# Kernel tuning notes

Measured on AMD Instinct MI355X. Metric: run time of the kernel, lower is better.

Reference implementation:

```python
import jax, jax.numpy as jnp
import numpy as np


def gcn_conv(x, src, dst, W, b, num_nodes):
    """PyG GCNConv: out = D^{-1/2} (A+I) D^{-1/2} X W + b (self-loops already in src/dst)."""
    h = x @ W  # [N, F_out]
    ones = jnp.ones(dst.shape[0], dtype=x.dtype)
    deg = jax.ops.segment_sum(ones, dst, num_segments=num_nodes)  # in-degree incl self-loop
    dis = jnp.where(deg > 0, jax.lax.rsqrt(deg), jnp.zeros_like(deg))  # deg^{-1/2}
    norm = dis[src] * dis[dst]  # [E]
    msg = h[src] * norm[:, None]  # gather + scale, [E, F_out]
    out = jax.ops.segment_sum(msg, dst, num_segments=num_nodes) + b
    return out


def setup_inputs() -> dict:
    key = jax.random.key(0)
    k = jax.random.split(key, 6)
    N, E, F_IN, HID, C = 100000, 3200000, 128, 16, 8
    x = jax.random.normal(k[0], (N, F_IN), dtype=jnp.float32)
    edge_index = jax.random.randint(k[1], (2, E), 0, N, dtype=jnp.int64)
    W1 = jax.random.normal(k[2], (F_IN, HID), dtype=jnp.float32) * (1.0 / np.sqrt(F_IN))
    b1 = jnp.zeros((HID,), dtype=jnp.float32)
    W2 = jax.random.normal(k[3], (HID, C), dtype=jnp.float32) * (1.0 / np.sqrt(HID))
    b2 = jnp.zeros((C,), dtype=jnp.float32)
    return {"x": x, "edge_index": edge_index, "W1": W1, "b1": b1, "W2": W2, "b2": b2}


def reference(x, edge_index, W1, b1, W2, b2):
    N = x.shape[0]
    loop = jnp.arange(N, dtype=edge_index.dtype)
    src = jnp.concatenate([edge_index[0], loop])  # add self-loops
    dst = jnp.concatenate([edge_index[1], loop])
    h = gcn_conv(x, src, dst, W1, b1, N)
    h = jax.nn.relu(h)  # dropout is identity in eval mode
    out = gcn_conv(h, src, dst, W2, b2, N)
    return out
```

## Files before the change

kernel.cpp:

```cpp
#include <hip/hip_runtime.h>
#include <hip/hip_fp16.h>

#define F_IN 128
#define HID 16
#define C_OUT 8
#define BSH 6
#define BSZ 64
#define G1 1024
#define NBMAX 1600
#define CAP 3072

typedef unsigned int uint;

__device__ inline int chunk_of_block(int blk) {
    return ((blk & 7) << 7) | (blk >> 3);
}

__global__ void count_kernel(const int* __restrict__ dst, uint* __restrict__ counts,
                             int E, int CE, int NB) {
    __shared__ uint h[NBMAX];
    int chunk = chunk_of_block(blockIdx.x), tid = threadIdx.x;
    for (int i = tid; i < NB; i += 256) h[i] = 0;
    __syncthreads();
    int base = chunk * CE, end = min(E, base + CE);
    int n = end - base;
    if (n > 0) {
        int n4 = n >> 2;
        const int4* p = reinterpret_cast<const int4*>(dst + base);
        for (int i = tid; i < n4; i += 256) {
            int4 d = p[i];
            atomicAdd(&h[((uint)d.x) >> BSH], 1u);
            atomicAdd(&h[((uint)d.y) >> BSH], 1u);
            atomicAdd(&h[((uint)d.z) >> BSH], 1u);
            atomicAdd(&h[((uint)d.w) >> BSH], 1u);
        }
        for (int i = base + (n4 << 2) + tid; i < end; i += 256)
            atomicAdd(&h[((uint)dst[i]) >> BSH], 1u);
    }
    __syncthreads();
    for (int i = tid; i < NB; i += 256)
        counts[(size_t)i * G1 + chunk] = h[i];
}

__global__ void scanA_kernel(uint* __restrict__ counts, uint* __restrict__ btot) {
    int b = blockIdx.x, tid = threadIdx.x;
    int lane = tid & 63, wid = tid >> 6;
    uint v = counts[(size_t)b * G1 + tid];
    uint inc = v;
#pragma unroll
    for (int o = 1; o < 64; o <<= 1) {
        uint t = __shfl_up(inc, o);
        if (lane >= o) inc += t;
    }
    __shared__ uint wsum[16];
    if (lane == 63) wsum[wid] = inc;
    __syncthreads();
    if (tid < 16) {
        uint w = wsum[tid], iw = w;
#pragma unroll
        for (int o = 1; o < 16; o <<= 1) {
            uint t = __shfl_up(iw, o);
            if (tid >= o) iw += t;
        }
        wsum[tid] = iw - w;
        if (tid == 15) btot[b] = iw;
    }
    __syncthreads();
    counts[(size_t)b * G1 + tid] = wsum[wid] + inc - v;
}

__global__ void scanB_kernel(const uint* __restrict__ btot, uint* __restrict__ bbase,
                             int NB, int E) {
    __shared__ uint wsum[4];
    __shared__ uint ctot;
    int tid = threadIdx.x, lane = tid & 63, wid = tid >> 6;
    uint base = 0;
    for (int c0 = 0; c0 < NB; c0 += 256) {
        int i = c0 + tid;
        uint v = (i < NB) ? btot[i] : 0u;
        uint inc = v;
#pragma unroll
        for (int o = 1; o < 64; o <<= 1) {
            uint t = __shfl_up(inc, o);
            if (lane >= o) inc += t;
        }
        if (lane == 63) wsum[wid] = inc;
        __syncthreads();
        if (tid == 0) {
            uint s = 0;
#pragma unroll
            for (int k = 0; k < 4; ++k) { uint t = wsum[k]; wsum[k] = s; s += t; }
            ctot = s;
        }
        __syncthreads();
        if (i < NB) bbase[i] = base + wsum[wid] + inc - v;
        base += ctot;
        __syncthreads();
    }
    if (tid == 0) bbase[NB] = (uint)E;
}

__global__ void place_kernel(const int* __restrict__ src, const int* __restrict__ dst,
                             const uint* __restrict__ offs, const uint* __restrict__ bbase,
                             uint* __restrict__ rec, int E, int CE, int NB) {
    __shared__ uint cur[NBMAX];
    int chunk = chunk_of_block(blockIdx.x), tid = threadIdx.x;
    for (int i = tid; i < NB; i += 256)
        cur[i] = bbase[i] + offs[(size_t)i * G1 + chunk];
    __syncthreads();
    int base = chunk * CE, end = min(E, base + CE);
    int n = end - base;
    if (n <= 0) return;
    int n4 = n >> 2;
    const int4* ps = reinterpret_cast<const int4*>(src + base);
    const int4* pd = reinterpret_cast<const int4*>(dst + base);
    for (int i = tid; i < n4; i += 256) {
        int4 s = ps[i];
        int4 d = pd[i];
        uint p0 = atomicAdd(&cur[((uint)d.x) >> BSH], 1u);
        rec[p0] = (uint)s.x | (((uint)d.x & (BSZ - 1)) << 17);
        uint p1 = atomicAdd(&cur[((uint)d.y) >> BSH], 1u);
        rec[p1] = (uint)s.y | (((uint)d.y & (BSZ - 1)) << 17);
        uint p2 = atomicAdd(&cur[((uint)d.z) >> BSH], 1u);
        rec[p2] = (uint)s.z | (((uint)d.z & (BSZ - 1)) << 17);
        uint p3 = atomicAdd(&cur[((uint)d.w) >> BSH], 1u);
        rec[p3] = (uint)s.w | (((uint)d.w & (BSZ - 1)) << 17);
    }
    for (int i = base + (n4 << 2) + tid; i < end; i += 256) {
        int d = dst[i];
        uint b = ((uint)d) >> BSH;
        uint p = atomicAdd(&cur[b], 1u);
        rec[p] = (uint)src[i] | (((uint)d & (BSZ - 1)) << 17);
    }
}

__global__ void sortdis_kernel(uint* __restrict__ rec, const uint* __restrict__ bbase,
                               uint* __restrict__ nstart, float* __restrict__ dis,
                               int N, int NB) {
    __shared__ uint tmp[CAP];
    __shared__ uint h[BSZ];
    __shared__ uint cur[BSZ];
    int b = blockIdx.x, tid = threadIdx.x;
    if (tid < BSZ) h[tid] = 0;
    uint s0 = bbase[b], s1 = bbase[b + 1];
    uint seg = min(s1 - s0, (uint)CAP);
    __syncthreads();
    for (uint i = tid; i < seg; i += 256) {
        uint r = rec[s0 + i];
        tmp[i] = r;
        atomicAdd(&h[(r >> 17) & (BSZ - 1)], 1u);
    }
    __syncthreads();
    if (tid < BSZ) {
        uint v = h[tid], inc = v;
#pragma unroll
        for (int o = 1; o < BSZ; o <<= 1) {
            uint t = __shfl_up(inc, o);
            if (tid >= o) inc += t;
        }
        uint excl = inc - v;
        cur[tid] = s0 + excl;
        int n = b * BSZ + tid;
        if (n < N) {
            nstart[n] = s0 + excl;
            dis[n] = rsqrtf((float)v + 1.0f);
        }
    }
    if (b == NB - 1 && tid == 0) nstart[N] = s1;
    __syncthreads();
    for (uint i = tid; i < seg; i += 256) {
        uint r = tmp[i];
        uint p = atomicAdd(&cur[(r >> 17) & (BSZ - 1)], 1u);
        rec[p] = r & 0x1FFFFu;
    }
}

__global__ void h1_kernel(const float* __restrict__ x, const float* __restrict__ W1,
                          const float* __restrict__ dis, __half* __restrict__ hs1, int N) {
    __shared__ float w[F_IN * HID];
    for (int t = threadIdx.x; t < F_IN * HID; t += blockDim.x) w[t] = W1[t];
    __syncthreads();
    int row = blockIdx.x * blockDim.x + threadIdx.x;
    if (row >= N) return;
    float acc[HID];
#pragma unroll
    for (int j = 0; j < HID; ++j) acc[j] = 0.f;
    const float4* xr = reinterpret_cast<const float4*>(x + (size_t)row * F_IN);
#pragma unroll 4
    for (int k4 = 0; k4 < F_IN / 4; ++k4) {
        float4 v = xr[k4];
        int k = k4 * 4;
#pragma unroll
        for (int j = 0; j < HID; ++j) {
            acc[j] += v.x * w[(k + 0) * HID + j] + v.y * w[(k + 1) * HID + j]
                    + v.z * w[(k + 2) * HID + j] + v.w * w[(k + 3) * HID + j];
        }
    }
    float d = dis[row];
    uint u[8];
#pragma unroll
    for (int p = 0; p < 8; ++p) {
        __half2 hh = __floats2half2_rn(acc[2 * p] * d, acc[2 * p + 1] * d);
        u[p] = *reinterpret_cast<uint*>(&hh);
    }
    uint4* o = reinterpret_cast<uint4*>(hs1 + ((size_t)row << 4));
    o[0] = make_uint4(u[0], u[1], u[2], u[3]);
    o[1] = make_uint4(u[4], u[5], u[6], u[7]);
}

__device__ inline void acc8(uint4 v, float* a) {
    float2 f;
    f = __half22float2(*reinterpret_cast<const __half2*>(&v.x)); a[0] += f.x; a[1] += f.y;
    f = __half22float2(*reinterpret_cast<const __half2*>(&v.y)); a[2] += f.x; a[3] += f.y;
    f = __half22float2(*reinterpret_cast<const __half2*>(&v.z)); a[4] += f.x; a[5] += f.y;
    f = __half22float2(*reinterpret_cast<const __half2*>(&v.w)); a[6] += f.x; a[7] += f.y;
}

__global__ void agg1_kernel(const uint* __restrict__ rec, const uint* __restrict__ nstart,
                            const __half* __restrict__ hs1, const float* __restrict__ dis,
                            const float* __restrict__ b1v, const float* __restrict__ W2,
                            float* __restrict__ hs2, int N) {
    __shared__ float w2s[HID * C_OUT];
    __shared__ float b1s[HID];
    int tid = threadIdx.x;
    if (tid < HID * C_OUT) w2s[tid] = W2[tid];
    if (tid < HID) b1s[tid] = b1v[tid];
    __syncthreads();
    int ldn = tid >> 1, q = tid & 1;
    int n = blockIdx.x * 128 + ldn;
    if (n >= N) return;
    uint e = nstart[n], en = nstart[n + 1];
    const uint4* hb = reinterpret_cast<const uint4*>(hs1) + q;
    float a[8];
#pragma unroll
    for (int j = 0; j < 8; ++j) a[j] = 0.f;
    while (e + 8 <= en) {
        uint i0 = __builtin_nontemporal_load(rec + e);
        uint i1 = __builtin_nontemporal_load(rec + e + 1);
        uint i2 = __builtin_nontemporal_load(rec + e + 2);
        uint i3 = __builtin_nontemporal_load(rec + e + 3);
        uint i4 = __builtin_nontemporal_load(rec + e + 4);
        uint i5 = __builtin_nontemporal_load(rec + e + 5);
        uint i6 = __builtin_nontemporal_load(rec + e + 6);
        uint i7 = __builtin_nontemporal_load(rec + e + 7);
        uint4 v0 = hb[(size_t)i0 << 1];
        uint4 v1 = hb[(size_t)i1 << 1];
        uint4 v2 = hb[(size_t)i2 << 1];
        uint4 v3 = hb[(size_t)i3 << 1];
        uint4 v4 = hb[(size_t)i4 << 1];
        uint4 v5 = hb[(size_t)i5 << 1];
        uint4 v6 = hb[(size_t)i6 << 1];
        uint4 v7 = hb[(size_t)i7 << 1];
        acc8(v0, a); acc8(v1, a); acc8(v2, a); acc8(v3, a);
        acc8(v4, a); acc8(v5, a); acc8(v6, a); acc8(v7, a);
        e += 8;
    }
    while (e < en) {
        uint i0 = __builtin_nontemporal_load(rec + e);
        uint4 v = hb[(size_t)i0 << 1];
        acc8(v, a);
        ++e;
    }
    uint4 sv = hb[(size_t)n << 1];
    float s[8];
    {
        float2 f;
        f = __half22float2(*reinterpret_cast<const __half2*>(&sv.x)); s[0] = f.x; s[1] = f.y;
        f = __half22float2(*reinterpret_cast<const __half2*>(&sv.y)); s[2] = f.x; s[3] = f.y;
        f = __half22float2(*reinterpret_cast<const __half2*>(&sv.z)); s[4] = f.x; s[5] = f.y;
        f = __half22float2(*reinterpret_cast<const __half2*>(&sv.w)); s[6] = f.x; s[7] = f.y;
    }
    float dv = dis[n];
    float r[8];
#pragma unroll
    for (int j = 0; j < 8; ++j)
        r[j] = fmaxf(dv * (a[j] + s[j]) + b1s[q * 8 + j], 0.f);
    float p[C_OUT];
#pragma unroll
    for (int c = 0; c < C_OUT; ++c) {
        float t = 0.f;
#pragma unroll
        for (int j = 0; j < 8; ++j) t += r[j] * w2s[(q * 8 + j) * C_OUT + c];
        p[c] = t;
    }
#pragma unroll
    for (int c = 0; c < C_OUT; ++c) p[c] += __shfl_xor(p[c], 1);
    float4 o;
    o.x = p[q * 4 + 0] * dv;
    o.y = p[q * 4 + 1] * dv;
    o.z = p[q * 4 + 2] * dv;
    o.w = p[q * 4 + 3] * dv;
    *reinterpret_cast<float4*>(hs2 + ((size_t)n << 3) + (q << 2)) = o;
}

__global__ void agg2_kernel(const uint* __restrict__ rec, const uint* __restrict__ nstart,
                            const float* __restrict__ hs2, const float* __restrict__ dis,
                            const float* __restrict__ b2v, float* __restrict__ out, int N) {
    int tid = threadIdx.x;
    int ldn = tid >> 1, q = tid & 1;
    int n = blockIdx.x * 128 + ldn;
    if (n >= N) return;
    uint e = nstart[n], en = nstart[n + 1];
    const float* hq = hs2 + (q << 2);
    float ax = 0.f, ay = 0.f, az = 0.f, aw = 0.f;
    while (e + 8 <= en) {
        uint i0 = __builtin_nontemporal_load(rec + e);
        uint i1 = __builtin_nontemporal_load(rec + e + 1);
        uint i2 = __builtin_nontemporal_load(rec + e + 2);
        uint i3 = __builtin_nontemporal_load(rec + e + 3);
        uint i4 = __builtin_nontemporal_load(rec + e + 4);
        uint i5 = __builtin_nontemporal_load(rec + e + 5);
        uint i6 = __builtin_nontemporal_load(rec + e + 6);
        uint i7 = __builtin_nontemporal_load(rec + e + 7);
        float4 v0 = *reinterpret_cast<const float4*>(hq + ((size_t)i0 << 3));
        float4 v1 = *reinterpret_cast<const float4*>(hq + ((size_t)i1 << 3));
        float4 v2 = *reinterpret_cast<const float4*>(hq + ((size_t)i2 << 3));
        float4 v3 = *reinterpret_cast<const float4*>(hq + ((size_t)i3 << 3));
        float4 v4 = *reinterpret_cast<const float4*>(hq + ((size_t)i4 << 3));
        float4 v5 = *reinterpret_cast<const float4*>(hq + ((size_t)i5 << 3));
        float4 v6 = *reinterpret_cast<const float4*>(hq + ((size_t)i6 << 3));
        float4 v7 = *reinterpret_cast<const float4*>(hq + ((size_t)i7 << 3));
        ax += ((v0.x + v1.x) + (v2.x + v3.x)) + ((v4.x + v5.x) + (v6.x + v7.x));
        ay += ((v0.y + v1.y) + (v2.y + v3.y)) + ((v4.y + v5.y) + (v6.y + v7.y));
        az += ((v0.z + v1.z) + (v2.z + v3.z)) + ((v4.z + v5.z) + (v6.z + v7.z));
        aw += ((v0.w + v1.w) + (v2.w + v3.w)) + ((v4.w + v5.w) + (v6.w + v7.w));
        e += 8;
    }
    while (e < en) {
        uint i0 = __builtin_nontemporal_load(rec + e);
        float4 v = *reinterpret_cast<const float4*>(hq + ((size_t)i0 << 3));
        ax += v.x; ay += v.y; az += v.z; aw += v.w;
        ++e;
    }
    float4 self = *reinterpret_cast<const float4*>(hq + ((size_t)n << 3));
    float dv = dis[n];
    float4 o;
    o.x = dv * (ax + self.x) + b2v[q * 4 + 0];
    o.y = dv * (ay + self.y) + b2v[q * 4 + 1];
    o.z = dv * (az + self.z) + b2v[q * 4 + 2];
    o.w = dv * (aw + self.w) + b2v[q * 4 + 3];
    *reinterpret_cast<float4*>(out + ((size_t)n << 3) + (q << 2)) = o;
}

extern "C" void kernel_launch(void* const* d_in, const int* in_sizes, int n_in,
                              void* d_out, int out_size, void* d_ws, size_t ws_size,
                              hipStream_t stream) {
    const float* x  = (const float*)d_in[0];
    const int*   ei = (const int*)d_in[1];
    const float* W1 = (const float*)d_in[2];
    const float* b1 = (const float*)d_in[3];
    const float* W2 = (const float*)d_in[4];
    const float* b2 = (const float*)d_in[5];
    float* out = (float*)d_out;

    int N = in_sizes[0] / F_IN;
    int E = in_sizes[1] / 2;
    const int* src = ei;
    const int* dst = ei + E;

    int NB = (N + BSZ - 1) / BSZ;
    int CE = (((E + G1 - 1) / G1) + 3) & ~3;

    float*  hs2   = (float*)d_ws;
    __half* hs1   = (__half*)(hs2 + (size_t)8 * N);
    float*  dis   = (float*)(hs2 + (size_t)16 * N);
    uint*   nstart = (uint*)(dis + N);
    uint*   rec   = nstart + N + 1;
    uint*   counts = rec + E;
    uint*   btot  = counts + (size_t)NB * G1;
    uint*   bbase = btot + NB;

    const int B = 256;
    count_kernel<<<G1, B, 0, stream>>>(dst, counts, E, CE, NB);
    scanA_kernel<<<NB, G1, 0, stream>>>(counts, btot);
    scanB_kernel<<<1, B, 0, stream>>>(btot, bbase, NB, E);
    place_kernel<<<G1, B, 0, stream>>>(src, dst, counts, bbase, rec, E, CE, NB);
    sortdis_kernel<<<NB, B, 0, stream>>>(rec, bbase, nstart, dis, N, NB);
    h1_kernel<<<(N + B - 1) / B, B, 0, stream>>>(x, W1, dis, hs1, N);
    agg1_kernel<<<(N + 127) / 128, B, 0, stream>>>(rec, nstart, hs1, dis, b1, W2, hs2, N);
    agg2_kernel<<<(N + 127) / 128, B, 0, stream>>>(rec, nstart, hs2, dis, b2, out, N);
}
```

Before: 160.3 us.

## Split node edge lists across two lanes and use wave-aggregated bin atomics in sort

```diff
diff --git a/kernel.cpp b/kernel.cpp
--- a/kernel.cpp
+++ b/kernel.cpp
@@ -141,16 +141,39 @@
     __shared__ uint h[BSZ];
     __shared__ uint cur[BSZ];
     int b = blockIdx.x, tid = threadIdx.x;
+    uint lane = (uint)(tid & 63);
     if (tid < BSZ) h[tid] = 0;
     uint s0 = bbase[b], s1 = bbase[b + 1];
     uint seg = min(s1 - s0, (uint)CAP);
     __syncthreads();
-    for (uint i = tid; i < seg; i += 256) {
+
+    uint hreg = 0;
+    uint i = (uint)tid;
+    uint wbase = (uint)(tid & ~63);
+    while (wbase + 64 <= seg) {
         uint r = rec[s0 + i];
         tmp[i] = r;
-        atomicAdd(&h[(r >> 17) & (BSZ - 1)], 1u);
-    }
-    __syncthreads();
+        uint bin = (r >> 17) & 63u;
+        unsigned long long bal[6];
+#pragma unroll
+        for (int bit = 0; bit < 6; ++bit)
+            bal[bit] = __ballot((bin >> bit) & 1u);
+        unsigned long long m = ~0ull;
+#pragma unroll
+        for (int bit = 0; bit < 6; ++bit)
+            m &= ((lane >> bit) & 1u) ? bal[bit] : ~bal[bit];
+        hreg += (uint)__popcll(m);
+        i += 256; wbase += 256;
+    }
+    while (i < seg) {
+        uint r = rec[s0 + i];
+        tmp[i] = r;
+        atomicAdd(&h[(r >> 17) & 63u], 1u);
+        i += 256;
+    }
+    if (hreg) atomicAdd(&h[lane], hreg);
+    __syncthreads();
+
     if (tid < BSZ) {
         uint v = h[tid], inc = v;
 #pragma unroll
@@ -168,10 +191,31 @@
     }
     if (b == NB - 1 && tid == 0) nstart[N] = s1;
     __syncthreads();
-    for (uint i = tid; i < seg; i += 256) {
+
+    i = (uint)tid;
+    wbase = (uint)(tid & ~63);
+    while (wbase + 64 <= seg) {
         uint r = tmp[i];
-        uint p = atomicAdd(&cur[(r >> 17) & (BSZ - 1)], 1u);
+        uint bin = (r >> 17) & 63u;
+        unsigned long long m = ~0ull;
+#pragma unroll
+        for (int bit = 0; bit < 6; ++bit) {
+            unsigned long long bal = __ballot((bin >> bit) & 1u);
+            m &= ((bin >> bit) & 1u) ? bal : ~bal;
+        }
+        uint leader = (uint)__ffsll((unsigned long long)m) - 1u;
+        uint rank = (uint)__popcll(m & ((1ull << lane) - 1ull));
+        uint basep = 0;
+        if (lane == leader) basep = atomicAdd(&cur[bin], (uint)__popcll(m));
+        basep = (uint)__shfl((int)basep, (int)leader);
+        rec[basep + rank] = r & 0x1FFFFu;
+        i += 256; wbase += 256;
+    }
+    while (i < seg) {
+        uint r = tmp[i];
+        uint p = atomicAdd(&cur[(r >> 17) & 63u], 1u);
         rec[p] = r & 0x1FFFFu;
+        i += 256;
     }
 }
 
@@ -226,23 +270,26 @@
     if (tid < HID * C_OUT) w2s[tid] = W2[tid];
     if (tid < HID) b1s[tid] = b1v[tid];
     __syncthreads();
-    int ldn = tid >> 1, q = tid & 1;
-    int n = blockIdx.x * 128 + ldn;
+    int ldn = tid >> 2;
+    uint q  = (uint)(tid & 1);
+    uint rr = (uint)((tid >> 1) & 1);
+    int n = blockIdx.x * 64 + ldn;
     if (n >= N) return;
     uint e = nstart[n], en = nstart[n + 1];
     const uint4* hb = reinterpret_cast<const uint4*>(hs1) + q;
     float a[8];
 #pragma unroll
     for (int j = 0; j < 8; ++j) a[j] = 0.f;
-    while (e + 8 <= en) {
-        uint i0 = __builtin_nontemporal_load(rec + e);
-        uint i1 = __builtin_nontemporal_load(rec + e + 1);
-        uint i2 = __builtin_nontemporal_load(rec + e + 2);
-        uint i3 = __builtin_nontemporal_load(rec + e + 3);
-        uint i4 = __builtin_nontemporal_load(rec + e + 4);
-        uint i5 = __builtin_nontemporal_load(rec + e + 5);
-        uint i6 = __builtin_nontemporal_load(rec + e + 6);
-        uint i7 = __builtin_nontemporal_load(rec + e + 7);
+    uint i = e + rr;
+    while (i + 14 < en) {
+        uint i0 = __builtin_nontemporal_load(rec + i);
+        uint i1 = __builtin_nontemporal_load(rec + i + 2);
+        uint i2 = __builtin_nontemporal_load(rec + i + 4);
+        uint i3 = __builtin_nontemporal_load(rec + i + 6);
+        uint i4 = __builtin_nontemporal_load(rec + i + 8);
+        uint i5 = __builtin_nontemporal_load(rec + i + 10);
+        uint i6 = __builtin_nontemporal_load(rec + i + 12);
+        uint i7 = __builtin_nontemporal_load(rec + i + 14);
         uint4 v0 = hb[(size_t)i0 << 1];
         uint4 v1 = hb[(size_t)i1 << 1];
         uint4 v2 = hb[(size_t)i2 << 1];
@@ -253,14 +300,16 @@
         uint4 v7 = hb[(size_t)i7 << 1];
         acc8(v0, a); acc8(v1, a); acc8(v2, a); acc8(v3, a);
         acc8(v4, a); acc8(v5, a); acc8(v6, a); acc8(v7, a);
-        e += 8;
-    }
-    while (e < en) {
-        uint i0 = __builtin_nontemporal_load(rec + e);
+        i += 16;
+    }
+    while (i < en) {
+        uint i0 = __builtin_nontemporal_load(rec + i);
         uint4 v = hb[(size_t)i0 << 1];
         acc8(v, a);
-        ++e;
-    }
+        i += 2;
+    }
+#pragma unroll
+    for (int j = 0; j < 8; ++j) a[j] += __shfl_xor(a[j], 2);
     uint4 sv = hb[(size_t)n << 1];
     float s[8];
     {
@@ -285,33 +334,38 @@
     }
 #pragma unroll
     for (int c = 0; c < C_OUT; ++c) p[c] += __shfl_xor(p[c], 1);
-    float4 o;
-    o.x = p[q * 4 + 0] * dv;
-    o.y = p[q * 4 + 1] * dv;
-    o.z = p[q * 4 + 2] * dv;
-    o.w = p[q * 4 + 3] * dv;
-    *reinterpret_cast<float4*>(hs2 + ((size_t)n << 3) + (q << 2)) = o;
+    if (rr == 0) {
+        float4 o;
+        o.x = p[q * 4 + 0] * dv;
+        o.y = p[q * 4 + 1] * dv;
+        o.z = p[q * 4 + 2] * dv;
+        o.w = p[q * 4 + 3] * dv;
+        *reinterpret_cast<float4*>(hs2 + ((size_t)n << 3) + (q << 2)) = o;
+    }
 }
 
 __global__ void agg2_kernel(const uint* __restrict__ rec, const uint* __restrict__ nstart,
                             const float* __restrict__ hs2, const float* __restrict__ dis,
                             const float* __restrict__ b2v, float* __restrict__ out, int N) {
     int tid = threadIdx.x;
-    int ldn = tid >> 1, q = tid & 1;
-    int n = blockIdx.x * 128 + ldn;
+    int ldn = tid >> 2;
+    uint q  = (uint)(tid & 1);
+    uint rr = (uint)((tid >> 1) & 1);
+    int n = blockIdx.x * 64 + ldn;
     if (n >= N) return;
     uint e = nstart[n], en = nstart[n + 1];
     const float* hq = hs2 + (q << 2);
     float ax = 0.f, ay = 0.f, az = 0.f, aw = 0.f;
-    while (e + 8 <= en) {
-        uint i0 = __builtin_nontemporal_load(rec + e);
-        uint i1 = __builtin_nontemporal_load(rec + e + 1);
-        uint i2 = __builtin_nontemporal_load(rec + e + 2);
-        uint i3 = __builtin_nontemporal_load(rec + e + 3);
-        uint i4 = __builtin_nontemporal_load(rec + e + 4);
-        uint i5 = __builtin_nontemporal_load(rec + e + 5);
-        uint i6 = __builtin_nontemporal_load(rec + e + 6);
-        uint i7 = __builtin_nontemporal_load(rec + e + 7);
+    uint i = e + rr;
+    while (i + 14 < en) {
+        uint i0 = __builtin_nontemporal_load(rec + i);
+        uint i1 = __builtin_nontemporal_load(rec + i + 2);
+        uint i2 = __builtin_nontemporal_load(rec + i + 4);
+        uint i3 = __builtin_nontemporal_load(rec + i + 6);
+        uint i4 = __builtin_nontemporal_load(rec + i + 8);
+        uint i5 = __builtin_nontemporal_load(rec + i + 10);
+        uint i6 = __builtin_nontemporal_load(rec + i + 12);
+        uint i7 = __builtin_nontemporal_load(rec + i + 14);
         float4 v0 = *reinterpret_cast<const float4*>(hq + ((size_t)i0 << 3));
         float4 v1 = *reinterpret_cast<const float4*>(hq + ((size_t)i1 << 3));
         float4 v2 = *reinterpret_cast<const float4*>(hq + ((size_t)i2 << 3));
@@ -324,22 +378,28 @@
         ay += ((v0.y + v1.y) + (v2.y + v3.y)) + ((v4.y + v5.y) + (v6.y + v7.y));
         az += ((v0.z + v1.z) + (v2.z + v3.z)) + ((v4.z + v5.z) + (v6.z + v7.z));
         aw += ((v0.w + v1.w) + (v2.w + v3.w)) + ((v4.w + v5.w) + (v6.w + v7.w));
-        e += 8;
-    }
-    while (e < en) {
-        uint i0 = __builtin_nontemporal_load(rec + e);
+        i += 16;
+    }
+    while (i < en) {
+        uint i0 = __builtin_nontemporal_load(rec + i);
         float4 v = *reinterpret_cast<const float4*>(hq + ((size_t)i0 << 3));
         ax += v.x; ay += v.y; az += v.z; aw += v.w;
-        ++e;
-    }
-    float4 self = *reinterpret_cast<const float4*>(hq + ((size_t)n << 3));
-    float dv = dis[n];
-    float4 o;
-    o.x = dv * (ax + self.x) + b2v[q * 4 + 0];
-    o.y = dv * (ay + self.y) + b2v[q * 4 + 1];
-    o.z = dv * (az + self.z) + b2v[q * 4 + 2];
-    o.w = dv * (aw + self.w) + b2v[q * 4 + 3];
-    *reinterpret_cast<float4*>(out + ((size_t)n << 3) + (q << 2)) = o;
+        i += 2;
+    }
+    ax += __shfl_xor(ax, 2);
+    ay += __shfl_xor(ay, 2);
+    az += __shfl_xor(az, 2);
+    aw += __shfl_xor(aw, 2);
+    if (rr == 0) {
+        float4 self = *reinterpret_cast<const float4*>(hq + ((size_t)n << 3));
+        float dv = dis[n];
+        float4 o;
+        o.x = dv * (ax + self.x) + b2v[q * 4 + 0];
+        o.y = dv * (ay + self.y) + b2v[q * 4 + 1];
+        o.z = dv * (az + self.z) + b2v[q * 4 + 2];
+        o.w = dv * (aw + self.w) + b2v[q * 4 + 3];
+        *reinterpret_cast<float4*>(out + ((size_t)n << 3) + (q << 2)) = o;
+    }
 }
 
 extern "C" void kernel_launch(void* const* d_in, const int* in_sizes, int n_in,
@@ -377,6 +437,6 @@
     place_kernel<<<G1, B, 0, stream>>>(src, dst, counts, bbase, rec, E, CE, NB);
     sortdis_kernel<<<NB, B, 0, stream>>>(rec, bbase, nstart, dis, N, NB);
     h1_kernel<<<(N + B - 1) / B, B, 0, stream>>>(x, W1, dis, hs1, N);
-    agg1_kernel<<<(N + 127) / 128, B, 0, stream>>>(rec, nstart, hs1, dis, b1, W2, hs2, N);
-    agg2_kernel<<<(N + 127) / 128, B, 0, stream>>>(rec, nstart, hs2, dis, b2, out, N);
-}
+    agg1_kernel<<<(N + 63) / 64, B, 0, stream>>>(rec, nstart, hs1, dis, b1, W2, hs2, N);
+    agg2_kernel<<<(N + 63) / 64, B, 0, stream>>>(rec, nstart, hs2, dis, b2, out, N);
+}
```

New measurement: 165.8 us. 1.03x slower.
